# Performance work log

Measured on AMD Instinct MI355X. Metric: run time of the kernel, lower is better.

The kernel has to match this reference:

```python
import jax, jax.numpy as jnp
import numpy as np

E, H, DQ, DV = 1024, 16, 64, 64
B, S = 8, 4096
EPS = 1e-5

def _ln(x, g, b):
    mu = jnp.mean(x, axis=-1, keepdims=True)
    var = jnp.mean((x - mu) ** 2, axis=-1, keepdims=True)
    return (x - mu) * jax.lax.rsqrt(var + EPS) * g + b

def setup_inputs() -> dict:
    key = jax.random.key(0)
    ks = jax.random.split(key, 10)
    s = lambda fan_in: 1.0 / np.sqrt(fan_in)
    return {
        "x": jax.random.normal(ks[0], (B, S, E), jnp.float32),
        "qk_w": jax.random.uniform(ks[1], (H * (DQ + DQ), E), jnp.float32, -s(E), s(E)),
        "qk_b": jax.random.uniform(ks[2], (H * (DQ + DQ),), jnp.float32, -s(E), s(E)),
        "v_w": jax.random.uniform(ks[3], (H * DV, E), jnp.float32, -s(E), s(E)),
        "v_b": jax.random.uniform(ks[4], (H * DV,), jnp.float32, -s(E), s(E)),
        "proj_w": jax.random.uniform(ks[5], (E, H * DV), jnp.float32, -s(H * DV), s(H * DV)),
        "proj_b": jax.random.uniform(ks[6], (E,), jnp.float32, -s(H * DV), s(H * DV)),
        "ff_w": jax.random.uniform(ks[7], (E, E), jnp.float32, -s(E), s(E)),
        "ff_b": jax.random.uniform(ks[8], (E,), jnp.float32, -s(E), s(E)),
        "ln_g": jnp.ones((E,), jnp.float32),
        "ln_b": jnp.zeros((E,), jnp.float32),
    }

def reference(x, qk_w, qk_b, v_w, v_b, proj_w, proj_b, ff_w, ff_b, ln_g, ln_b):
    b, s, _ = x.shape
    qk = (x @ qk_w.T + qk_b).reshape(b, s, 2, H, DQ)
    q, k = qk[:, :, 0], qk[:, :, 1]              # [B,S,H,DQ] each
    v = (x @ v_w.T + v_b).reshape(b, s, H, DV)   # [B,S,H,DV]
    # NOTE: faithful to source — attention is over the HEAD axis per position.
    attn = jnp.einsum('bshd,bsgd->bshg', q, k) / np.sqrt(DQ).astype(np.float32)
    attn = jax.nn.softmax(attn, axis=-1)         # [B,S,H,H]
    x_ = jnp.einsum('bshg,bsgd->bshd', attn, v).reshape(b, s, H * DV)
    x_ = x_ @ proj_w.T + proj_b
    out = _ln(x_ + x, ln_g, ln_b)
    out = out @ ff_w.T + ff_b
    out = jax.nn.gelu(out, approximate=False)
    out = _ln(out + x, ln_g, ln_b)
    return out
```

## Files before the change

kernel.cpp:

```cpp
#include <hip/hip_runtime.h>
#include <cstdint>
#include <cstddef>

typedef unsigned short u16;
typedef unsigned int   u32;

using short8 = __attribute__((ext_vector_type(8))) short;
using f32x4  = __attribute__((ext_vector_type(4))) float;

#define M_TOK 32768
#define E_DIM 1024
#define NQKV  3072

__device__ __forceinline__ u16 f2bf(float f) {
  u32 u = __float_as_uint(f);
  u += 0x7FFFu + ((u >> 16) & 1u);
  return (u16)(u >> 16);
}
__device__ __forceinline__ float bf2f(u16 v) {
  return __uint_as_float((u32)v << 16);
}
__device__ __forceinline__ u32 pack2(float a, float b) {
  return (u32)f2bf(a) | ((u32)f2bf(b) << 16);
}

__device__ __forceinline__ void gl_lds16(const void* g, void* l) {
  __builtin_amdgcn_global_load_lds(
      (const __attribute__((address_space(1))) u32*)g,
      (__attribute__((address_space(3))) u32*)l, 16, 0, 0);
}

__global__ __launch_bounds__(256) void cast_all_k(
    const float4* __restrict__ x,
    const float4* __restrict__ qkw, const float4* __restrict__ vw,
    const float4* __restrict__ pw,  const float4* __restrict__ fw,
    const float4* __restrict__ qkb, const float4* __restrict__ vb,
    uint2* __restrict__ xb,
    uint2* __restrict__ wqkv, uint2* __restrict__ wproj, uint2* __restrict__ wff,
    float4* __restrict__ qkvbias) {
  const int gid = blockIdx.x * 256 + threadIdx.x;
  if (gid < 8388608) {
    const float4 v = x[gid];
    xb[gid] = make_uint2(pack2(v.x, v.y), pack2(v.z, v.w));
    return;
  }
  const int w = gid - 8388608;
  float4 v; uint2* dst; int di;
  if (w < 524288)        { v = qkw[w];           dst = wqkv;  di = w; }
  else if (w < 786432)   { v = vw[w - 524288];   dst = wqkv;  di = w; }
  else if (w < 1048576)  { v = pw[w - 786432];   dst = wproj; di = w - 786432; }
  else                   { v = fw[w - 1048576];  dst = wff;   di = w - 1048576; }
  dst[di] = make_uint2(pack2(v.x, v.y), pack2(v.z, v.w));
  if (w < 768) qkvbias[w] = (w < 512) ? qkb[w] : vb[w - 512];
}

template<int MODE>
__global__ __launch_bounds__(512, 2)
void gemm_bt(const u16* __restrict__ A, const u16* __restrict__ Bw,
             const float* __restrict__ bias, const u16* __restrict__ xres,
             u16* __restrict__ C, int M, int N, int K) {
  __shared__ __align__(16) u16 As[2][256 * 64];
  __shared__ __align__(16) u16 Bs[2][256 * 64];
  const int tid  = threadIdx.x;
  const int lane = tid & 63;
  const int wave = tid >> 6;
  const int wm = wave & 1;
  const int wn = wave >> 1;
  const int quad = lane >> 4;
  const int l15  = lane & 15;
  const int row0 = blockIdx.y * 256;
  const int col0 = blockIdx.x * 256;

  f32x4 acc[8][4];
  #pragma unroll
  for (int i = 0; i < 8; ++i)
    #pragma unroll
    for (int j = 0; j < 4; ++j)
      acc[i][j] = (f32x4){0.f, 0.f, 0.f, 0.f};

  const int rsub = tid >> 3;
  const int kch  = tid & 7;
  const int ck0 = quad ^ (l15 & 7);
  const int ck1 = (4 + quad) ^ (l15 & 7);
  const int mB = wm * 128 + l15;
  const int nB = wn * 64 + l15;

  auto STAGE_HALF = [&](const u16* __restrict__ src, int growbase, int kt,
                        u16* ldsTile, int half) {
    const int kel = kt << 6;
    #pragma unroll
    for (int c = 0; c < 2; ++c) {
      const int rl = c * 64 + rsub;
      const u16* g = src + (size_t)(growbase + half * 128 + rl) * K
                         + kel + ((kch ^ (rl & 7)) << 3);
      gl_lds16(g, ldsTile + (size_t)((half << 10) + (c << 9) + (wave << 6)) * 8);
    }
  };

  auto LDA4 = [&](short8 (&dst)[4][2], const u16* tile, int hh) {
    #pragma unroll
    for (int i = 0; i < 4; ++i) {
      const int m = mB + hh * 64 + i * 16;
      dst[i][0] = *(const short8*)(tile + m * 64 + ck0 * 8);
      dst[i][1] = *(const short8*)(tile + m * 64 + ck1 * 8);
    }
  };
  auto LDB2 = [&](short8 (&dst)[2][2], const u16* tile, int jj) {
    #pragma unroll
    for (int j = 0; j < 2; ++j) {
      const int n = nB + (jj + j) * 16;
      dst[j][0] = *(const short8*)(tile + n * 64 + ck0 * 8);
      dst[j][1] = *(const short8*)(tile + n * 64 + ck1 * 8);
    }
  };
  auto QUAD = [&](short8 (&af)[4][2], short8 (&bf)[2][2], int i0, int j0) {
    #pragma unroll
    for (int kk = 0; kk < 2; ++kk)
      #pragma unroll
      for (int i = 0; i < 4; ++i)
        #pragma unroll
        for (int j = 0; j < 2; ++j)
          acc[i0 + i][j0 + j] = __builtin_amdgcn_mfma_f32_16x16x32_bf16(
              af[i][kk], bf[j][kk], acc[i0 + i][j0 + j], 0, 0, 0);
  };

  const int NT = K >> 6;
  const int NITER = NT >> 1;

  STAGE_HALF(A,  row0, 0, As[0], 0);
  STAGE_HALF(A,  row0, 0, As[0], 1);
  STAGE_HALF(Bw, col0, 0, Bs[0], 0);
  STAGE_HALF(Bw, col0, 0, Bs[0], 1);
  STAGE_HALF(A,  row0, 1, As[1], 0);
  STAGE_HALF(A,  row0, 1, As[1], 1);
  asm volatile("s_waitcnt vmcnt(4)" ::: "memory");
  __builtin_amdgcn_s_barrier();
  __builtin_amdgcn_sched_barrier(0);

  short8 aLo[4][2], aHi[4][2], bLo[2][2], bHi[2][2];

  for (int it = 0; it < NITER; ++it) {
    #pragma unroll
    for (int h = 0; h < 2; ++h) {
      const int tB = 2 * it + h + 1;
      const int tA = 2 * it + h + 2;
      const int ktB = (tB >= NT) ? tB - NT : tB;
      const int ktA = (tA >= NT) ? tA - NT : tA;
      const u16* AsR = As[h];
      const u16* BsR = Bs[h];
      u16* BsW = Bs[h ^ 1];
      u16* AsW = As[h];

      LDA4(aLo, AsR, 0);
      LDB2(bLo, BsR, 0);
      STAGE_HALF(Bw, col0, ktB, BsW, 0);
      __builtin_amdgcn_s_barrier();
      asm volatile("s_waitcnt lgkmcnt(0)" ::: "memory");
      __builtin_amdgcn_sched_barrier(0);
      __builtin_amdgcn_s_setprio(1);
      QUAD(aLo, bLo, 0, 0);
      __builtin_amdgcn_s_setprio(0);
      __builtin_amdgcn_s_barrier();
      __builtin_amdgcn_sched_barrier(0);

      LDA4(aHi, AsR, 1);
      STAGE_HALF(Bw, col0, ktB, BsW, 1);
      __builtin_amdgcn_s_barrier();
      asm volatile("s_waitcnt lgkmcnt(0)" ::: "memory");
      __builtin_amdgcn_sched_barrier(0);
      __builtin_amdgcn_s_setprio(1);
      QUAD(aHi, bLo, 4, 0);
      __builtin_amdgcn_s_setprio(0);
      __builtin_amdgcn_s_barrier();
      __builtin_amdgcn_sched_barrier(0);

      LDB2(bHi, BsR, 2);
      STAGE_HALF(A, row0, ktA, AsW, 0);
      __builtin_amdgcn_s_barrier();
      asm volatile("s_waitcnt lgkmcnt(0)" ::: "memory");
      __builtin_amdgcn_sched_barrier(0);
      __builtin_amdgcn_s_setprio(1);
      QUAD(aLo, bHi, 0, 2);
      __builtin_amdgcn_s_setprio(0);
      __builtin_amdgcn_s_barrier();
      __builtin_amdgcn_sched_barrier(0);

      STAGE_HALF(A, row0, ktA, AsW, 1);
      __builtin_amdgcn_s_barrier();
      asm volatile("s_waitcnt lgkmcnt(0)" ::: "memory");
      __builtin_amdgcn_sched_barrier(0);
      __builtin_amdgcn_s_setprio(1);
      QUAD(aHi, bHi, 4, 2);
      __builtin_amdgcn_s_setprio(0);
      asm volatile("s_waitcnt vmcnt(4)" ::: "memory");
      __builtin_amdgcn_s_barrier();
      __builtin_amdgcn_sched_barrier(0);
    }
  }
  asm volatile("s_waitcnt vmcnt(0)" ::: "memory");

  #pragma unroll
  for (int j = 0; j < 4; ++j) {
    const int col = col0 + wn * 64 + j * 16 + l15;
    const float bj = bias[col];
    #pragma unroll
    for (int ai = 0; ai < 8; ++ai) {
      const int rowb = row0 + wm * 128 + ai * 16 + quad * 4;
      #pragma unroll
      for (int r = 0; r < 4; ++r) {
        const int row = rowb + r;
        float v = acc[ai][j][r] + bj;
        if (MODE == 1) {
          v += bf2f(xres[(size_t)row * N + col]);
        } else if (MODE == 2) {
          v = 0.5f * v * (1.0f + erff(v * 0.70710678118654752f))
              + bf2f(xres[(size_t)row * N + col]);
        }
        C[(size_t)row * N + col] = f2bf(v);
      }
    }
  }
}

__global__ __launch_bounds__(256)
void attn_k(const u16* __restrict__ qkv, u16* __restrict__ ao) {
  __shared__ __align__(16) u16 pb[4][256];
  const int tid  = threadIdx.x;
  const int wave = tid >> 6;
  const int lane = tid & 63;
  const int quad = lane >> 4;
  const int l15  = lane & 15;
  const int t = blockIdx.x * 4 + wave;
  const u16* base = qkv + (size_t)t * 3072;
  const u16* qb = base;
  const u16* kb = base + 1024;
  const u16* vb = base + 2048;

  const int fo = l15 * 64 + quad * 8;
  const short8 a0 = *(const short8*)(qb + fo);
  const short8 a1 = *(const short8*)(qb + fo + 32);
  const short8 b0 = *(const short8*)(kb + fo);
  const short8 b1 = *(const short8*)(kb + fo + 32);
  f32x4 s = (f32x4){0.f, 0.f, 0.f, 0.f};
  s = __builtin_amdgcn_mfma_f32_16x16x32_bf16(a0, b0, s, 0, 0, 0);
  s = __builtin_amdgcn_mfma_f32_16x16x32_bf16(a1, b1, s, 0, 0, 0);

  float rinv[4];
  float ev[4];
  #pragma unroll
  for (int r = 0; r < 4; ++r) {
    float sv = s[r] * 0.125f;
    float m = sv;
    m = fmaxf(m, __shfl_xor(m, 1));
    m = fmaxf(m, __shfl_xor(m, 2));
    m = fmaxf(m, __shfl_xor(m, 4));
    m = fmaxf(m, __shfl_xor(m, 8));
    const float e = __expf(sv - m);
    float sm = e;
    sm += __shfl_xor(sm, 1);
    sm += __shfl_xor(sm, 2);
    sm += __shfl_xor(sm, 4);
    sm += __shfl_xor(sm, 8);
    ev[r] = e;
    rinv[r] = 1.0f / sm;
  }

  u16* pw = pb[wave];
  #pragma unroll
  for (int r = 0; r < 4; ++r)
    pw[(quad * 4 + r) * 16 + l15] = f2bf(ev[r]);

  short8 pa = (short8){0, 0, 0, 0, 0, 0, 0, 0};
  if (quad < 2)
    pa = *(const short8*)(pw + l15 * 16 + quad * 8);

  f32x4 o[4];
  #pragma unroll
  for (int nt = 0; nt < 4; ++nt) o[nt] = (f32x4){0.f, 0.f, 0.f, 0.f};
  #pragma unroll
  for (int nt = 0; nt < 4; ++nt) {
    short8 vf = (short8){0, 0, 0, 0, 0, 0, 0, 0};
    if (quad < 2) {
      #pragma unroll
      for (int j = 0; j < 8; ++j)
        vf[j] = (short)vb[(quad * 8 + j) * 64 + nt * 16 + l15];
    }
    o[nt] = __builtin_amdgcn_mfma_f32_16x16x32_bf16(pa, vf, o[nt], 0, 0, 0);
  }

  u16* aop = ao + (size_t)t * 1024;
  #pragma unroll
  for (int nt = 0; nt < 4; ++nt)
    #pragma unroll
    for (int r = 0; r < 4; ++r)
      aop[(quad * 4 + r) * 64 + nt * 16 + l15] = f2bf(o[nt][r] * rinv[r]);
}

template<int F32OUT>
__global__ __launch_bounds__(256)
void ln_k(const u16* __restrict__ s, const float* __restrict__ gw,
          const float* __restrict__ bw, void* __restrict__ outp) {
  const int row = blockIdx.x;
  const int tid = threadIdx.x;
  const uint2 u = ((const uint2*)(s + (size_t)row * 1024))[tid];
  const float v0 = __uint_as_float(u.x << 16);
  const float v1 = __uint_as_float(u.x & 0xFFFF0000u);
  const float v2 = __uint_as_float(u.y << 16);
  const float v3 = __uint_as_float(u.y & 0xFFFF0000u);
  float sum = v0 + v1 + v2 + v3;
  float sq  = v0 * v0 + v1 * v1 + v2 * v2 + v3 * v3;
  #pragma unroll
  for (int off = 32; off >= 1; off >>= 1) {
    sum += __shfl_xor(sum, off);
    sq  += __shfl_xor(sq, off);
  }
  __shared__ float red[8];
  const int wave = tid >> 6;
  if ((tid & 63) == 0) { red[wave] = sum; red[4 + wave] = sq; }
  __syncthreads();
  sum = red[0] + red[1] + red[2] + red[3];
  sq  = red[4] + red[5] + red[6] + red[7];
  const float mu   = sum * (1.0f / 1024.0f);
  const float rstd = rsqrtf(sq * (1.0f / 1024.0f) - mu * mu + 1e-5f);
  const float4 g4 = ((const float4*)gw)[tid];
  const float4 b4 = ((const float4*)bw)[tid];
  const float o0 = (v0 - mu) * rstd * g4.x + b4.x;
  const float o1 = (v1 - mu) * rstd * g4.y + b4.y;
  const float o2 = (v2 - mu) * rstd * g4.z + b4.z;
  const float o3 = (v3 - mu) * rstd * g4.w + b4.w;
  if (F32OUT) {
    ((float4*)outp)[(size_t)row * 256 + tid] = make_float4(o0, o1, o2, o3);
  } else {
    ((uint2*)outp)[(size_t)row * 256 + tid] = make_uint2(pack2(o0, o1), pack2(o2, o3));
  }
}

extern "C" void kernel_launch(void* const* d_in, const int* in_sizes, int n_in,
                              void* d_out, int out_size, void* d_ws, size_t ws_size,
                              hipStream_t stream) {
  const float* x      = (const float*)d_in[0];
  const float* qk_w   = (const float*)d_in[1];
  const float* qk_b   = (const float*)d_in[2];
  const float* v_w    = (const float*)d_in[3];
  const float* v_b    = (const float*)d_in[4];
  const float* proj_w = (const float*)d_in[5];
  const float* proj_b = (const float*)d_in[6];
  const float* ff_w   = (const float*)d_in[7];
  const float* ff_b   = (const float*)d_in[8];
  const float* ln_g   = (const float*)d_in[9];
  const float* ln_b   = (const float*)d_in[10];

  char* ws = (char*)d_ws;
  u16*   wqkv    = (u16*)(ws);
  u16*   wproj   = (u16*)(ws + 6291456);
  u16*   wff     = (u16*)(ws + 8388608);
  float* qkvbias = (float*)(ws + 10485760);
  u16*   qkv     = (u16*)(ws + 10498048);
  u16*   s1      = qkv;
  u16*   s2      = (u16*)(ws + 10498048 + 67108864);
  u16*   ao      = (u16*)(ws + 211824640);
  u16*   h1      = ao;
  u16*   xb      = (u16*)(ws + 278933504);

  cast_all_k<<<37888, 256, 0, stream>>>(
      (const float4*)x,
      (const float4*)qk_w, (const float4*)v_w, (const float4*)proj_w, (const float4*)ff_w,
      (const float4*)qk_b, (const float4*)v_b,
      (uint2*)xb, (uint2*)wqkv, (uint2*)wproj, (uint2*)wff, (float4*)qkvbias);

  dim3 gqkv(NQKV / 256, M_TOK / 256);
  gemm_bt<0><<<gqkv, 512, 0, stream>>>(xb, wqkv, qkvbias, nullptr, qkv, M_TOK, NQKV, E_DIM);

  attn_k<<<M_TOK / 4, 256, 0, stream>>>(qkv, ao);

  dim3 gsq(E_DIM / 256, M_TOK / 256);
  gemm_bt<1><<<gsq, 512, 0, stream>>>(ao, wproj, proj_b, xb, s1, M_TOK, E_DIM, E_DIM);

  ln_k<0><<<M_TOK, 256, 0, stream>>>(s1, ln_g, ln_b, h1);

  gemm_bt<2><<<gsq, 512, 0, stream>>>(h1, wff, ff_b, xb, s2, M_TOK, E_DIM, E_DIM);

  ln_k<1><<<M_TOK, 256, 0, stream>>>(s2, ln_g, ln_b, d_out);
}
```

Before: 949.3 us.

## Replace pipelined 256x256 GEMM with simple single-buffered 128x256 tile kernel

Rewrites the bf16 GEMM to use 128x256 output tiles with a single LDS buffer per operand and a plain load-sync-compute loop. This drops the hand-scheduled double-buffered pipeline with its priority and scheduling barriers. The launch-bounds minimum-blocks hint rises from two to four per CU, aiming for more resident waves and lower register pressure through smaller accumulators. In exchange it gives up overlap of global loads with MFMA work and lowers data reuse per tile, so global traffic rises.

```diff
diff --git a/kernel.cpp b/kernel.cpp
--- a/kernel.cpp
+++ b/kernel.cpp
@@ -55,12 +55,12 @@
 }
 
 template<int MODE>
-__global__ __launch_bounds__(512, 2)
+__global__ __launch_bounds__(512, 4)
 void gemm_bt(const u16* __restrict__ A, const u16* __restrict__ Bw,
              const float* __restrict__ bias, const u16* __restrict__ xres,
              u16* __restrict__ C, int M, int N, int K) {
-  __shared__ __align__(16) u16 As[2][256 * 64];
-  __shared__ __align__(16) u16 Bs[2][256 * 64];
+  __shared__ __align__(16) u16 As[128 * 64];
+  __shared__ __align__(16) u16 Bs[256 * 64];
   const int tid  = threadIdx.x;
   const int lane = tid & 63;
   const int wave = tid >> 6;
@@ -68,148 +68,62 @@
   const int wn = wave >> 1;
   const int quad = lane >> 4;
   const int l15  = lane & 15;
-  const int row0 = blockIdx.y * 256;
+  const int row0 = blockIdx.y * 128;
   const int col0 = blockIdx.x * 256;
 
-  f32x4 acc[8][4];
-  #pragma unroll
-  for (int i = 0; i < 8; ++i)
+  f32x4 acc[4][4];
+  #pragma unroll
+  for (int i = 0; i < 4; ++i)
     #pragma unroll
     for (int j = 0; j < 4; ++j)
       acc[i][j] = (f32x4){0.f, 0.f, 0.f, 0.f};
 
-  const int rsub = tid >> 3;
-  const int kch  = tid & 7;
-  const int ck0 = quad ^ (l15 & 7);
-  const int ck1 = (4 + quad) ^ (l15 & 7);
-  const int mB = wm * 128 + l15;
-  const int nB = wn * 64 + l15;
-
-  auto STAGE_HALF = [&](const u16* __restrict__ src, int growbase, int kt,
-                        u16* ldsTile, int half) {
-    const int kel = kt << 6;
-    #pragma unroll
-    for (int c = 0; c < 2; ++c) {
-      const int rl = c * 64 + rsub;
-      const u16* g = src + (size_t)(growbase + half * 128 + rl) * K
-                         + kel + ((kch ^ (rl & 7)) << 3);
-      gl_lds16(g, ldsTile + (size_t)((half << 10) + (c << 9) + (wave << 6)) * 8);
-    }
-  };
-
-  auto LDA4 = [&](short8 (&dst)[4][2], const u16* tile, int hh) {
-    #pragma unroll
-    for (int i = 0; i < 4; ++i) {
-      const int m = mB + hh * 64 + i * 16;
-      dst[i][0] = *(const short8*)(tile + m * 64 + ck0 * 8);
-      dst[i][1] = *(const short8*)(tile + m * 64 + ck1 * 8);
-    }
-  };
-  auto LDB2 = [&](short8 (&dst)[2][2], const u16* tile, int jj) {
-    #pragma unroll
-    for (int j = 0; j < 2; ++j) {
-      const int n = nB + (jj + j) * 16;
-      dst[j][0] = *(const short8*)(tile + n * 64 + ck0 * 8);
-      dst[j][1] = *(const short8*)(tile + n * 64 + ck1 * 8);
-    }
-  };
-  auto QUAD = [&](short8 (&af)[4][2], short8 (&bf)[2][2], int i0, int j0) {
-    #pragma unroll
-    for (int kk = 0; kk < 2; ++kk)
+  const int ml_t = tid >> 3;
+  const int gch  = (tid & 7) ^ (ml_t & 7);
+  const u16* srcA0 = A  + (size_t)(row0 + ml_t) * K + gch * 8;
+  const u16* srcB0 = Bw + (size_t)(col0 + ml_t) * K + gch * 8;
+  const int ldsbase = wave * 512;
+
+  const int nkt = K >> 6;
+  for (int kt = 0; kt < nkt; ++kt) {
+    const int k0 = kt << 6;
+    __syncthreads();
+    gl_lds16(srcA0 + k0,                     As + ldsbase);
+    gl_lds16(srcA0 + k0 + (size_t)64 * K,    As + ldsbase + 4096);
+    #pragma unroll
+    for (int c = 0; c < 4; ++c)
+      gl_lds16(srcB0 + k0 + (size_t)c * 64 * K, Bs + ldsbase + c * 4096);
+    __syncthreads();
+    #pragma unroll
+    for (int kk = 0; kk < 2; ++kk) {
+      const int cidx = (kk << 2) + quad;
+      short8 af[4], bfr[4];
+      #pragma unroll
+      for (int i = 0; i < 4; ++i) {
+        const int m = wm * 64 + i * 16 + l15;
+        af[i]  = *(const short8*)(As + (m * 8 + (cidx ^ (m & 7))) * 8);
+        const int n = wn * 64 + i * 16 + l15;
+        bfr[i] = *(const short8*)(Bs + (n * 8 + (cidx ^ (n & 7))) * 8);
+      }
       #pragma unroll
       for (int i = 0; i < 4; ++i)
         #pragma unroll
-        for (int j = 0; j < 2; ++j)
-          acc[i0 + i][j0 + j] = __builtin_amdgcn_mfma_f32_16x16x32_bf16(
-              af[i][kk], bf[j][kk], acc[i0 + i][j0 + j], 0, 0, 0);
-  };
-
-  const int NT = K >> 6;
-  const int NITER = NT >> 1;
-
-  STAGE_HALF(A,  row0, 0, As[0], 0);
-  STAGE_HALF(A,  row0, 0, As[0], 1);
-  STAGE_HALF(Bw, col0, 0, Bs[0], 0);
-  STAGE_HALF(Bw, col0, 0, Bs[0], 1);
-  STAGE_HALF(A,  row0, 1, As[1], 0);
-  STAGE_HALF(A,  row0, 1, As[1], 1);
-  asm volatile("s_waitcnt vmcnt(4)" ::: "memory");
-  __builtin_amdgcn_s_barrier();
-  __builtin_amdgcn_sched_barrier(0);
-
-  short8 aLo[4][2], aHi[4][2], bLo[2][2], bHi[2][2];
-
-  for (int it = 0; it < NITER; ++it) {
-    #pragma unroll
-    for (int h = 0; h < 2; ++h) {
-      const int tB = 2 * it + h + 1;
-      const int tA = 2 * it + h + 2;
-      const int ktB = (tB >= NT) ? tB - NT : tB;
-      const int ktA = (tA >= NT) ? tA - NT : tA;
-      const u16* AsR = As[h];
-      const u16* BsR = Bs[h];
-      u16* BsW = Bs[h ^ 1];
-      u16* AsW = As[h];
-
-      LDA4(aLo, AsR, 0);
-      LDB2(bLo, BsR, 0);
-      STAGE_HALF(Bw, col0, ktB, BsW, 0);
-      __builtin_amdgcn_s_barrier();
-      asm volatile("s_waitcnt lgkmcnt(0)" ::: "memory");
-      __builtin_amdgcn_sched_barrier(0);
-      __builtin_amdgcn_s_setprio(1);
-      QUAD(aLo, bLo, 0, 0);
-      __builtin_amdgcn_s_setprio(0);
-      __builtin_amdgcn_s_barrier();
-      __builtin_amdgcn_sched_barrier(0);
-
-      LDA4(aHi, AsR, 1);
-      STAGE_HALF(Bw, col0, ktB, BsW, 1);
-      __builtin_amdgcn_s_barrier();
-      asm volatile("s_waitcnt lgkmcnt(0)" ::: "memory");
-      __builtin_amdgcn_sched_barrier(0);
-      __builtin_amdgcn_s_setprio(1);
-      QUAD(aHi, bLo, 4, 0);
-      __builtin_amdgcn_s_setprio(0);
-      __builtin_amdgcn_s_barrier();
-      __builtin_amdgcn_sched_barrier(0);
-
-      LDB2(bHi, BsR, 2);
-      STAGE_HALF(A, row0, ktA, AsW, 0);
-      __builtin_amdgcn_s_barrier();
-      asm volatile("s_waitcnt lgkmcnt(0)" ::: "memory");
-      __builtin_amdgcn_sched_barrier(0);
-      __builtin_amdgcn_s_setprio(1);
-      QUAD(aLo, bHi, 0, 2);
-      __builtin_amdgcn_s_setprio(0);
-      __builtin_amdgcn_s_barrier();
-      __builtin_amdgcn_sched_barrier(0);
-
-      STAGE_HALF(A, row0, ktA, AsW, 1);
-      __builtin_amdgcn_s_barrier();
-      asm volatile("s_waitcnt lgkmcnt(0)" ::: "memory");
-      __builtin_amdgcn_sched_barrier(0);
-      __builtin_amdgcn_s_setprio(1);
-      QUAD(aHi, bHi, 4, 2);
-      __builtin_amdgcn_s_setprio(0);
-      asm volatile("s_waitcnt vmcnt(4)" ::: "memory");
-      __builtin_amdgcn_s_barrier();
-      __builtin_amdgcn_sched_barrier(0);
+        for (int j = 0; j < 4; ++j)
+          acc[i][j] = __builtin_amdgcn_mfma_f32_16x16x32_bf16(af[i], bfr[j], acc[i][j], 0, 0, 0);
     }
   }
-  asm volatile("s_waitcnt vmcnt(0)" ::: "memory");
 
   #pragma unroll
   for (int j = 0; j < 4; ++j) {
     const int col = col0 + wn * 64 + j * 16 + l15;
     const float bj = bias[col];
     #pragma unroll
-    for (int ai = 0; ai < 8; ++ai) {
-      const int rowb = row0 + wm * 128 + ai * 16 + quad * 4;
+    for (int i = 0; i < 4; ++i) {
+      const int rowb = row0 + wm * 64 + i * 16 + quad * 4;
       #pragma unroll
       for (int r = 0; r < 4; ++r) {
         const int row = rowb + r;
-        float v = acc[ai][j][r] + bj;
+        float v = acc[i][j][r] + bj;
         if (MODE == 1) {
           v += bf2f(xres[(size_t)row * N + col]);
         } else if (MODE == 2) {
@@ -368,12 +282,12 @@
       (const float4*)qk_b, (const float4*)v_b,
       (uint2*)xb, (uint2*)wqkv, (uint2*)wproj, (uint2*)wff, (float4*)qkvbias);
 
-  dim3 gqkv(NQKV / 256, M_TOK / 256);
+  dim3 gqkv(NQKV / 256, M_TOK / 128);
   gemm_bt<0><<<gqkv, 512, 0, stream>>>(xb, wqkv, qkvbias, nullptr, qkv, M_TOK, NQKV, E_DIM);
 
   attn_k<<<M_TOK / 4, 256, 0, stream>>>(qkv, ao);
 
-  dim3 gsq(E_DIM / 256, M_TOK / 256);
+  dim3 gsq(E_DIM / 256, M_TOK / 128);
   gemm_bt<1><<<gsq, 512, 0, stream>>>(ao, wproj, proj_b, xb, s1, M_TOK, E_DIM, E_DIM);
 
   ln_k<0><<<M_TOK, 256, 0, stream>>>(s1, ln_g, ln_b, h1);
```

Measured after the change: 837.0 us. 1.13x faster.
